# Optimization experiments

Measured on AMD Instinct MI355X. Metric: run time of the kernel, lower is better.

## Reference

```python
import jax, jax.numpy as jnp
import numpy as np

K_SIZE = 5  # must match init_kwargs


def _local_attention(main, ref, ref_value, k_size=K_SIZE):
    """k x k windowed dot-product attention ('dot' mode of RefLocal).

    main:      [B,H,W,C] queries
    ref:       [B,H,W,C] keys (zero-padded SAME, matching extract_volume_patches)
    ref_value: [B,H,W,V] values
    Zero padding contributes logit 0 (NOT -inf), faithful to TF SAME padding.
    """
    p = (k_size - 1) // 2
    B, H, W, C = main.shape
    ref_p = jnp.pad(ref, ((0, 0), (p, p), (p, p), (0, 0)))
    val_p = jnp.pad(ref_value, ((0, 0), (p, p), (p, p), (0, 0)))

    offsets = [(i, j) for i in range(k_size) for j in range(k_size)]
    # logits[b,h,w,idx] = <main[b,h,w,:], ref shifted by offset idx>
    logits = jnp.stack(
        [jnp.einsum('bhwc,bhwc->bhw', main, ref_p[:, i:i + H, j:j + W, :])
         for (i, j) in offsets], axis=-1)  # [B,H,W,k*k]
    attn = jax.nn.softmax(logits, axis=-1)

    out = jnp.zeros(ref_value.shape, dtype=ref_value.dtype)
    for idx, (i, j) in enumerate(offsets):
        out = out + attn[..., idx][..., None] * val_p[:, i:i + H, j:j + W, :]
    return out  # [B,H,W,V]


def setup_inputs() -> dict:
    key = jax.random.key(0)
    k1, k2, k3 = jax.random.split(key, 3)
    B, H, W, C, V = 8, 96, 96, 192, 96
    return {
        'main': jax.random.normal(k1, (B, H, W, C), dtype=jnp.float32),
        'ref': jax.random.normal(k2, (B, H, W, C), dtype=jnp.float32),
        'ref_value': jax.random.normal(k3, (B, H, W, V), dtype=jnp.float32),
    }


def reference(main, ref, ref_value):
    return _local_attention(main, ref, ref_value, K_SIZE)
```

## Files before the change

### kernel.cpp

```cpp
#include <hip/hip_runtime.h>


#define BATCH 8
#define HH 96
#define WW 96
#define CH 192
#define VV 96
#define KS 5
#define PAD 2
#define TH 8
#define TW 8
#define HT (TH + 2 * PAD)
#define WT (TW + 2 * PAD)
#define NPIX (HT * WT)
#define CHUNK 32
#define SPX 36
#define RSTR 101
#define SO 33
#define SOFF (NPIX * SPX)
#define SSZ (SOFF + 64 * SO)

__global__ __launch_bounds__(256, 2) void reflocal_kernel(
    const float* __restrict__ qry, const float* __restrict__ key,
    const float* __restrict__ val, float* __restrict__ out) {
  int braw = blockIdx.x;
  int L = (braw & 7) * 144 + (braw >> 3);
  int bb = L / 144;
  int t2 = L - bb * 144;
  int tyy = t2 / 12;
  int txx = t2 - tyy * 12;
  int h0 = tyy * TH, w0 = txx * TW;

  int tid = threadIdx.x;
  int g = tid >> 6;
  int p = tid & 63;
  int ty = p >> 3, tx = p & 7;
  int h = h0 + ty, w = w0 + tx;

  __shared__ float s[SSZ];

  int q4 = (tid & 7) * 4;
  int pidx[5];
  int ldst[5];
#pragma unroll
  for (int r = 0; r < 5; ++r) {
    int px = (tid >> 3) + 32 * r;
    if (px < NPIX) {
      int ry = px / WT, rx = px - ry * WT;
      int hh = h0 - PAD + ry, ww = w0 - PAD + rx;
      pidx[r] = ((unsigned)hh < HH && (unsigned)ww < WW)
                    ? (bb * HH + hh) * WW + ww
                    : -1;
      ldst[r] = px * SPX + q4;
    } else {
      pidx[r] = -2;
      ldst[r] = 0;
    }
  }

  float lg[25];
#pragma unroll
  for (int o = 0; o < 25; ++o) lg[o] = 0.f;

  const float* qbase = qry + (size_t)((bb * HH + h) * WW + w) * CH;

  float4 pf[5];
#pragma unroll
  for (int r = 0; r < 5; ++r) {
    float4 v4 = make_float4(0.f, 0.f, 0.f, 0.f);
    if (pidx[r] >= 0)
      v4 = *(const float4*)(key + (size_t)pidx[r] * CH + q4);
    pf[r] = v4;
  }

  for (int c0 = 0; c0 < CH; c0 += CHUNK) {
    __syncthreads();
#pragma unroll
    for (int r = 0; r < 5; ++r)
      if (pidx[r] != -2) *(float4*)(&s[ldst[r]]) = pf[r];
    __syncthreads();
    if (c0 + CHUNK < CH) {
      int cn = c0 + CHUNK + q4;
#pragma unroll
      for (int r = 0; r < 5; ++r) {
        float4 v4 = make_float4(0.f, 0.f, 0.f, 0.f);
        if (pidx[r] >= 0)
          v4 = *(const float4*)(key + (size_t)pidx[r] * CH + cn);
        pf[r] = v4;
      }
    }

    float4 m0 = *(const float4*)(qbase + c0 + g * 8);
    float4 m1 = *(const float4*)(qbase + c0 + g * 8 + 4);
#pragma unroll
    for (int i = 0; i < KS; ++i) {
#pragma unroll
      for (int j = 0; j < KS; ++j) {
        const float* sp = &s[((ty + i) * WT + tx + j) * SPX + g * 8];
        float4 k0 = *(const float4*)(sp);
        float4 k1 = *(const float4*)(sp + 4);
        lg[i * 5 + j] += m0.x * k0.x + m0.y * k0.y + m0.z * k0.z +
                         m0.w * k0.w + m1.x * k1.x + m1.y * k1.y +
                         m1.z * k1.z + m1.w * k1.w;
      }
    }
  }

  __syncthreads();
#pragma unroll
  for (int o = 0; o < 25; ++o) s[p * RSTR + g * 25 + o] = lg[o];
  __syncthreads();
#pragma unroll
  for (int o = 0; o < 25; ++o) {
    float v = s[p * RSTR + o];
#pragma unroll
    for (int g2 = 1; g2 < 4; ++g2) v += s[p * RSTR + g2 * 25 + o];
    lg[o] = v;
  }

#pragma unroll
  for (int r = 0; r < 5; ++r) {
    float4 v4 = make_float4(0.f, 0.f, 0.f, 0.f);
    if (pidx[r] >= 0)
      v4 = *(const float4*)(val + (size_t)pidx[r] * VV + q4);
    pf[r] = v4;
  }

  float mx = lg[0];
#pragma unroll
  for (int o = 1; o < 25; ++o) mx = fmaxf(mx, lg[o]);
  float sum = 0.f;
#pragma unroll
  for (int o = 0; o < 25; ++o) {
    lg[o] = __expf(lg[o] - mx);
    sum += lg[o];
  }
  float inv = 1.f / sum;
#pragma unroll
  for (int o = 0; o < 25; ++o) lg[o] *= inv;

  for (int v0 = 0; v0 < VV; v0 += CHUNK) {
    __syncthreads();
#pragma unroll
    for (int r = 0; r < 5; ++r)
      if (pidx[r] != -2) *(float4*)(&s[ldst[r]]) = pf[r];
    __syncthreads();
    if (v0 + CHUNK < VV) {
      int vn = v0 + CHUNK + q4;
#pragma unroll
      for (int r = 0; r < 5; ++r) {
        float4 v4 = make_float4(0.f, 0.f, 0.f, 0.f);
        if (pidx[r] >= 0)
          v4 = *(const float4*)(val + (size_t)pidx[r] * VV + vn);
        pf[r] = v4;
      }
    }

    float4 a0 = make_float4(0.f, 0.f, 0.f, 0.f);
    float4 a1 = make_float4(0.f, 0.f, 0.f, 0.f);
#pragma unroll
    for (int i = 0; i < KS; ++i) {
#pragma unroll
      for (int j = 0; j < KS; ++j) {
        const float* sp = &s[((ty + i) * WT + tx + j) * SPX + g * 8];
        float a = lg[i * 5 + j];
        float4 v0r = *(const float4*)(sp);
        float4 v1r = *(const float4*)(sp + 4);
        a0.x += a * v0r.x; a0.y += a * v0r.y;
        a0.z += a * v0r.z; a0.w += a * v0r.w;
        a1.x += a * v1r.x; a1.y += a * v1r.y;
        a1.z += a * v1r.z; a1.w += a * v1r.w;
      }
    }
    *(float4*)(&s[SOFF + p * SO + g * 8]) = a0;
    *(float4*)(&s[SOFF + p * SO + g * 8 + 4]) = a1;
    __syncthreads();

    for (int t = tid; t < 64 * (CHUNK / 4); t += 256) {
      int px = t >> 3, c4 = (t & 7) * 4;
      int pty = px >> 3, ptx = px & 7;
      float4 v4 = *(const float4*)(&s[SOFF + px * SO + c4]);
      *(float4*)(out + (size_t)((bb * HH + h0 + pty) * WW + w0 + ptx) * VV +
                 v0 + c4) = v4;
    }
  }
}

extern "C" void kernel_launch(void* const* d_in, const int* in_sizes, int n_in,
                              void* d_out, int out_size, void* d_ws,
                              size_t ws_size, hipStream_t stream) {
  const float* qry = (const float*)d_in[0];
  const float* key = (const float*)d_in[1];
  const float* val = (const float*)d_in[2];
  float* out = (float*)d_out;

  dim3 grid(BATCH * (HH / TH) * (WW / TW));
  dim3 block(256);
  reflocal_kernel<<<grid, block, 0, stream>>>(qry, key, val, out);
}
```

Measured before the change: 189.2 us.

## Assign two adjacent pixels per thread with sliding-window LDS reuse and shuffle reduction

Threads are remapped so each one handles two horizontally adjacent pixels over a 4-channel slice, instead of one pixel over an 8-channel slice. Each row loads 6 key/value vectors from LDS once and reuses them across both pixels' 5 window taps, which cuts LDS read traffic. The cross-thread channel reduction of logits now uses warp shuffles instead of an LDS round trip with extra barriers. Occupancy is raised to 3 blocks per SM, at the cost of doubled logit registers (50 accumulators) and more shuffle instructions.

Result: slower. 414.3 us (+119.0%).

```diff
diff --git a/kernel.cpp b/kernel.cpp
--- a/kernel.cpp
+++ b/kernel.cpp
@@ -15,12 +15,14 @@
 #define NPIX (HT * WT)
 #define CHUNK 32
 #define SPX 36
-#define RSTR 101
-#define SO 33
+#define SO 36
 #define SOFF (NPIX * SPX)
 #define SSZ (SOFF + 64 * SO)
 
-__global__ __launch_bounds__(256, 2) void reflocal_kernel(
+#define DOT4(m, k) \
+  ((m).x * (k).x + (m).y * (k).y + (m).z * (k).z + (m).w * (k).w)
+
+__global__ __launch_bounds__(256, 3) void reflocal_kernel(
     const float* __restrict__ qry, const float* __restrict__ key,
     const float* __restrict__ val, float* __restrict__ out) {
   int braw = blockIdx.x;
@@ -32,14 +34,13 @@
   int h0 = tyy * TH, w0 = txx * TW;
 
   int tid = threadIdx.x;
-  int g = tid >> 6;
-  int p = tid & 63;
-  int ty = p >> 3, tx = p & 7;
-  int h = h0 + ty, w = w0 + tx;
+  int s4 = (tid & 7) * 4;
+  int pr = (tid >> 3) >> 2;
+  int pc = (tid >> 3) & 3;
+  int qx0 = 2 * pc;
 
   __shared__ float s[SSZ];
 
-  int q4 = (tid & 7) * 4;
   int pidx[5];
   int ldst[5];
 #pragma unroll
@@ -51,25 +52,27 @@
       pidx[r] = ((unsigned)hh < HH && (unsigned)ww < WW)
                     ? (bb * HH + hh) * WW + ww
                     : -1;
-      ldst[r] = px * SPX + q4;
+      ldst[r] = px * SPX + s4;
     } else {
       pidx[r] = -2;
       ldst[r] = 0;
     }
   }
 
-  float lg[25];
-#pragma unroll
-  for (int o = 0; o < 25; ++o) lg[o] = 0.f;
-
-  const float* qbase = qry + (size_t)((bb * HH + h) * WW + w) * CH;
+  float lg0[25], lg1[25];
+#pragma unroll
+  for (int o = 0; o < 25; ++o) { lg0[o] = 0.f; lg1[o] = 0.f; }
+
+  const float* qb0 =
+      qry + (size_t)((bb * HH + h0 + pr) * WW + w0 + qx0) * CH;
+  const float* qb1 = qb0 + CH;
 
   float4 pf[5];
 #pragma unroll
   for (int r = 0; r < 5; ++r) {
     float4 v4 = make_float4(0.f, 0.f, 0.f, 0.f);
     if (pidx[r] >= 0)
-      v4 = *(const float4*)(key + (size_t)pidx[r] * CH + q4);
+      v4 = *(const float4*)(key + (size_t)pidx[r] * CH + s4);
     pf[r] = v4;
   }
 
@@ -80,7 +83,7 @@
       if (pidx[r] != -2) *(float4*)(&s[ldst[r]]) = pf[r];
     __syncthreads();
     if (c0 + CHUNK < CH) {
-      int cn = c0 + CHUNK + q4;
+      int cn = c0 + CHUNK + s4;
 #pragma unroll
       for (int r = 0; r < 5; ++r) {
         float4 v4 = make_float4(0.f, 0.f, 0.f, 0.f);
@@ -90,54 +93,68 @@
       }
     }
 
-    float4 m0 = *(const float4*)(qbase + c0 + g * 8);
-    float4 m1 = *(const float4*)(qbase + c0 + g * 8 + 4);
+    float4 m0 = *(const float4*)(qb0 + c0 + s4);
+    float4 m1 = *(const float4*)(qb1 + c0 + s4);
 #pragma unroll
     for (int i = 0; i < KS; ++i) {
+      const float* sp = &s[((pr + i) * WT + qx0) * SPX + s4];
+      float4 kr[6];
+#pragma unroll
+      for (int u = 0; u < 6; ++u) kr[u] = *(const float4*)(sp + u * SPX);
 #pragma unroll
       for (int j = 0; j < KS; ++j) {
-        const float* sp = &s[((ty + i) * WT + tx + j) * SPX + g * 8];
-        float4 k0 = *(const float4*)(sp);
-        float4 k1 = *(const float4*)(sp + 4);
-        lg[i * 5 + j] += m0.x * k0.x + m0.y * k0.y + m0.z * k0.z +
-                         m0.w * k0.w + m1.x * k1.x + m1.y * k1.y +
-                         m1.z * k1.z + m1.w * k1.w;
-      }
-    }
-  }
-
-  __syncthreads();
-#pragma unroll
-  for (int o = 0; o < 25; ++o) s[p * RSTR + g * 25 + o] = lg[o];
-  __syncthreads();
+        lg0[i * 5 + j] += DOT4(m0, kr[j]);
+        lg1[i * 5 + j] += DOT4(m1, kr[j + 1]);
+      }
+    }
+  }
+
 #pragma unroll
   for (int o = 0; o < 25; ++o) {
-    float v = s[p * RSTR + o];
-#pragma unroll
-    for (int g2 = 1; g2 < 4; ++g2) v += s[p * RSTR + g2 * 25 + o];
-    lg[o] = v;
+    lg0[o] += __shfl_xor(lg0[o], 1);
+    lg0[o] += __shfl_xor(lg0[o], 2);
+    lg0[o] += __shfl_xor(lg0[o], 4);
+    lg1[o] += __shfl_xor(lg1[o], 1);
+    lg1[o] += __shfl_xor(lg1[o], 2);
+    lg1[o] += __shfl_xor(lg1[o], 4);
   }
 
 #pragma unroll
   for (int r = 0; r < 5; ++r) {
     float4 v4 = make_float4(0.f, 0.f, 0.f, 0.f);
     if (pidx[r] >= 0)
-      v4 = *(const float4*)(val + (size_t)pidx[r] * VV + q4);
+      v4 = *(const float4*)(val + (size_t)pidx[r] * VV + s4);
     pf[r] = v4;
   }
 
-  float mx = lg[0];
-#pragma unroll
-  for (int o = 1; o < 25; ++o) mx = fmaxf(mx, lg[o]);
-  float sum = 0.f;
-#pragma unroll
-  for (int o = 0; o < 25; ++o) {
-    lg[o] = __expf(lg[o] - mx);
-    sum += lg[o];
-  }
-  float inv = 1.f / sum;
-#pragma unroll
-  for (int o = 0; o < 25; ++o) lg[o] *= inv;
+  {
+    float mx = lg0[0];
+#pragma unroll
+    for (int o = 1; o < 25; ++o) mx = fmaxf(mx, lg0[o]);
+    float sum = 0.f;
+#pragma unroll
+    for (int o = 0; o < 25; ++o) {
+      lg0[o] = __expf(lg0[o] - mx);
+      sum += lg0[o];
+    }
+    float inv = 1.f / sum;
+#pragma unroll
+    for (int o = 0; o < 25; ++o) lg0[o] *= inv;
+  }
+  {
+    float mx = lg1[0];
+#pragma unroll
+    for (int o = 1; o < 25; ++o) mx = fmaxf(mx, lg1[o]);
+    float sum = 0.f;
+#pragma unroll
+    for (int o = 0; o < 25; ++o) {
+      lg1[o] = __expf(lg1[o] - mx);
+      sum += lg1[o];
+    }
+    float inv = 1.f / sum;
+#pragma unroll
+    for (int o = 0; o < 25; ++o) lg1[o] *= inv;
+  }
 
   for (int v0 = 0; v0 < VV; v0 += CHUNK) {
     __syncthreads();
@@ -146,7 +163,7 @@
       if (pidx[r] != -2) *(float4*)(&s[ldst[r]]) = pf[r];
     __syncthreads();
     if (v0 + CHUNK < VV) {
-      int vn = v0 + CHUNK + q4;
+      int vn = v0 + CHUNK + s4;
 #pragma unroll
       for (int r = 0; r < 5; ++r) {
         float4 v4 = make_float4(0.f, 0.f, 0.f, 0.f);
@@ -160,20 +177,23 @@
     float4 a1 = make_float4(0.f, 0.f, 0.f, 0.f);
 #pragma unroll
     for (int i = 0; i < KS; ++i) {
+      const float* sp = &s[((pr + i) * WT + qx0) * SPX + s4];
+      float4 vr[6];
+#pragma unroll
+      for (int u = 0; u < 6; ++u) vr[u] = *(const float4*)(sp + u * SPX);
 #pragma unroll
       for (int j = 0; j < KS; ++j) {
-        const float* sp = &s[((ty + i) * WT + tx + j) * SPX + g * 8];
-        float a = lg[i * 5 + j];
-        float4 v0r = *(const float4*)(sp);
-        float4 v1r = *(const float4*)(sp + 4);
-        a0.x += a * v0r.x; a0.y += a * v0r.y;
-        a0.z += a * v0r.z; a0.w += a * v0r.w;
-        a1.x += a * v1r.x; a1.y += a * v1r.y;
-        a1.z += a * v1r.z; a1.w += a * v1r.w;
-      }
-    }
-    *(float4*)(&s[SOFF + p * SO + g * 8]) = a0;
-    *(float4*)(&s[SOFF + p * SO + g * 8 + 4]) = a1;
+        float w0a = lg0[i * 5 + j];
+        float w1a = lg1[i * 5 + j];
+        a0.x += w0a * vr[j].x;     a0.y += w0a * vr[j].y;
+        a0.z += w0a * vr[j].z;     a0.w += w0a * vr[j].w;
+        a1.x += w1a * vr[j + 1].x; a1.y += w1a * vr[j + 1].y;
+        a1.z += w1a * vr[j + 1].z; a1.w += w1a * vr[j + 1].w;
+      }
+    }
+    int px0 = pr * 8 + qx0;
+    *(float4*)(&s[SOFF + px0 * SO + s4]) = a0;
+    *(float4*)(&s[SOFF + (px0 + 1) * SO + s4]) = a1;
     __syncthreads();
 
     for (int t = tid; t < 64 * (CHUNK / 4); t += 256) {
```
